# Performance work log

Hardware: AMD Instinct MI355X
Metric: run time of the kernel (lower is better)

Reference implementation:

```python
import jax, jax.numpy as jnp
import numpy as np

DECAY = 0.85          # decay_factor
LAM = 0.5             # lambda_diversity
EPS = 1e-12


def setup_inputs() -> dict:
    key = jax.random.key(0)
    ks = jax.random.split(key, 6)
    N, D = 32768, 512
    return {
        "predictions": jax.random.normal(ks[0], (N,), jnp.float32),
        "target_scores": jax.random.normal(ks[1], (N,), jnp.float32),
        "context_embeddings": jax.random.normal(ks[2], (N, D), jnp.float32),
        "input_embeddings": jax.random.normal(ks[3], (N, D), jnp.float32),
        "dsm_embeddings": jax.random.normal(ks[4], (N, D), jnp.float32),
        "explanation_embeddings": jax.random.normal(ks[5], (N, D), jnp.float32),
        "k": 16,
    }


def reference(predictions, target_scores, context_embeddings, input_embeddings,
              dsm_embeddings, explanation_embeddings, k):
    # relevance probabilities over all N candidates (dim=0 softmax as in torch)
    rel = jax.nn.softmax(predictions.squeeze(), axis=0)

    # L2-normalize once so cos_sim is a plain dot product
    E = explanation_embeddings
    En = E / (jnp.linalg.norm(E, axis=-1, keepdims=True) + EPS)  # [N, D]
    N = En.shape[0]

    # Greedy ERR/MMR relevance-diversity selection of k items:
    #   score_t(i) = decay^t * rel[i] - lambda * max_{j in selected} cos(E_i, E_j)
    # pick argmax over unselected; err_score_t = decay^t * rel[selected_t]
    def step(carry, t):
        mask, max_sim = carry                       # [N] bool, [N] f32
        decay = DECAY ** t.astype(rel.dtype)
        score = decay * rel - LAM * max_sim
        score = jnp.where(mask, -jnp.inf, score)
        idx = jnp.argmax(score)
        err = rel[idx] * decay
        sim_new = En @ En[idx]                      # cos sim of all to new pick
        return (mask.at[idx].set(True),
                jnp.maximum(max_sim, sim_new)), (err, idx)

    init = (jnp.zeros((N,), bool), jnp.zeros((N,), rel.dtype))
    _, (errs, sel) = jax.lax.scan(step, init, jnp.arange(k))

    err_loss = -jnp.sum(errs)

    # mmr_loss = -sum_i max_j cos(E_i, E_j) over selected set (self included,
    # exactly as the original code does with util.cos_sim(...).max())
    S = En[sel]                                    # [k, D]
    sims = S @ S.T                                 # [k, k]
    mmr_loss = -jnp.sum(jnp.max(sims, axis=1))

    return err_loss + LAM * mmr_loss
```

## Files before the change

kernel.cpp:

```cpp
#include <hip/hip_runtime.h>
#include <cmath>


#define DECAYF 0.85f
#define LAMF   0.5f
#define EPSF   1e-12f

constexpr int D    = 512;
constexpr int KMAX = 16;
constexpr int NBLK = 256;
constexpr int TPB  = 1024;
constexpr int NW   = TPB / 64;
constexpr int RPW  = 8;
constexpr int RPB  = NW * RPW;

using u32 = unsigned int;
using u64 = unsigned long long;

__device__ inline float wsum(float v) {
#pragma unroll
    for (int o = 32; o > 0; o >>= 1) v += __shfl_xor(v, o);
    return v;
}
__device__ inline float wmaxf(float v) {
#pragma unroll
    for (int o = 32; o > 0; o >>= 1) v = fmaxf(v, __shfl_xor(v, o));
    return v;
}
__device__ inline u64 wmax64(u64 v) {
#pragma unroll
    for (int o = 32; o > 0; o >>= 1) {
        u64 w = __shfl_xor(v, o);
        v = (w > v) ? w : v;
    }
    return v;
}
__device__ inline u32 fkey(float f) {
    u32 u = __float_as_uint(f);
    return (u & 0x80000000u) ? ~u : (u | 0x80000000u);
}
__device__ inline u64 aload(const u64* p) {
    return __hip_atomic_load(p, __ATOMIC_RELAXED, __HIP_MEMORY_SCOPE_AGENT);
}
__device__ inline u64 poll_slot(const u64* p) {
    u64 v = aload(p);
    while (v == 0ull) { __builtin_amdgcn_s_sleep(1); v = aload(p); }
    return v;
}
__device__ inline void publish(u64* p, u64 v) {
    __hip_atomic_store(p, v, __ATOMIC_RELAXED, __HIP_MEMORY_SCOPE_AGENT);
}

__global__ __launch_bounds__(TPB, 4) void fused_kernel(
        const float* __restrict__ pred,
        const float* __restrict__ E,
        const int*   __restrict__ kptr,
        float* __restrict__ out,
        u64*   __restrict__ sm,
        u64*   __restrict__ part,
        int    SL) {
    const int b = blockIdx.x, tid = threadIdx.x;
    const int wv = tid >> 6, lane = tid & 63;

    __shared__ float pred_s[RPB];
    __shared__ u64   scan_s[NBLK];
    __shared__ u64   wkey_s[NW];
    __shared__ float m_s, S_s;
    __shared__ int   j_s;
    __shared__ int   sel_s[KMAX];
    __shared__ float invsel_s[KMAX];
    __shared__ float rmax_s[KMAX];

    int kk = kptr[0];
    if (kk > KMAX) kk = KMAX;
    if (kk < 0) kk = 0;

    if (tid < RPB) pred_s[tid] = pred[b * RPB + tid];
    __syncthreads();
    if (wv == 0) {
        float p0 = pred_s[lane], p1 = pred_s[lane + 64];
        float mb = wmaxf(fmaxf(p0, p1));
        float sb = wsum(expf(p0 - mb) + expf(p1 - mb));
        if (lane == 0)
            publish(&sm[(size_t)b * SL],
                    ((u64)__float_as_uint(mb) << 32) | __float_as_uint(sb));
    }
    asm volatile("" ::: "memory");

    const int row0 = b * RPB + wv * RPW;
    float r[RPW][8];
#pragma unroll
    for (int rr = 0; rr < RPW; ++rr) {
        const float4* p = (const float4*)(E + (size_t)(row0 + rr) * D) + 2 * lane;
        float4 a0 = p[0], a1 = p[1];
        r[rr][0] = a0.x; r[rr][1] = a0.y; r[rr][2] = a0.z; r[rr][3] = a0.w;
        r[rr][4] = a1.x; r[rr][5] = a1.y; r[rr][6] = a1.z; r[rr][7] = a1.w;
        float ss = 0.f;
#pragma unroll
        for (int e = 0; e < 8; ++e) ss += r[rr][e] * r[rr][e];
        ss = wsum(ss);
        float inv = 1.f / (sqrtf(ss) + EPSF);
#pragma unroll
        for (int e = 0; e < 8; ++e) r[rr][e] *= inv;
        asm volatile("" : "+v"(r[rr][0]), "+v"(r[rr][1]), "+v"(r[rr][2]), "+v"(r[rr][3]),
                          "+v"(r[rr][4]), "+v"(r[rr][5]), "+v"(r[rr][6]), "+v"(r[rr][7]));
    }

    if (tid < NBLK) scan_s[tid] = poll_slot(&sm[(size_t)tid * SL]);
    __syncthreads();
    if (wv == 0) {
        u64 v0 = scan_s[lane], v1 = scan_s[lane + 64],
            v2 = scan_s[lane + 128], v3 = scan_s[lane + 192];
        float m0 = __uint_as_float((u32)(v0 >> 32)), m1 = __uint_as_float((u32)(v1 >> 32));
        float m2 = __uint_as_float((u32)(v2 >> 32)), m3 = __uint_as_float((u32)(v3 >> 32));
        float M = wmaxf(fmaxf(fmaxf(m0, m1), fmaxf(m2, m3)));
        float acc = __uint_as_float((u32)(v0 & 0xFFFFFFFFull)) * expf(m0 - M)
                  + __uint_as_float((u32)(v1 & 0xFFFFFFFFull)) * expf(m1 - M)
                  + __uint_as_float((u32)(v2 & 0xFFFFFFFFull)) * expf(m2 - M)
                  + __uint_as_float((u32)(v3 & 0xFFFFFFFFull)) * expf(m3 - M);
        acc = wsum(acc);
        if (lane == 0) { m_s = M; S_s = acc; }
    }
    __syncthreads();
    const float M    = m_s;
    const float Sinv = 1.f / S_s;

    float drel_r[RPW], msim_r[RPW];
#pragma unroll
    for (int rr = 0; rr < RPW; ++rr) {
        drel_r[rr] = expf(pred_s[wv * RPW + rr] - M) * Sinv;
        msim_r[rr] = 0.f;
    }

    int j = -1;
    for (int t = 0; t < KMAX; ++t) {
        if (t >= kk) break;
        if (t > 0) {
            const float4* pj = (const float4*)(E + (size_t)j * D) + 2 * lane;
            float4 b0 = pj[0], b1 = pj[1];
            float bj[8] = {b0.x, b0.y, b0.z, b0.w, b1.x, b1.y, b1.z, b1.w};
            float ss = 0.f;
#pragma unroll
            for (int e = 0; e < 8; ++e) ss += bj[e] * bj[e];
            ss = wsum(ss);
            const float js = 1.f / (sqrtf(ss) + EPSF);
#pragma unroll
            for (int e = 0; e < 8; ++e) bj[e] *= js;
#pragma unroll
            for (int rr = 0; rr < RPW; ++rr) {
                float d = 0.f;
#pragma unroll
                for (int e = 0; e < 8; ++e) d += r[rr][e] * bj[e];
                d = wsum(d);
                msim_r[rr] = (row0 + rr == j) ? INFINITY
                                              : fmaxf(msim_r[rr], d);
            }
        }
        u64 best = 0ull;
#pragma unroll
        for (int rr = 0; rr < RPW; ++rr) {
            const float sc = drel_r[rr] - LAMF * msim_r[rr];
            const u64 key = ((u64)fkey(sc) << 32) | (u32)~(u32)(row0 + rr);
            best = (key > best) ? key : best;
        }
#pragma unroll
        for (int rr = 0; rr < RPW; ++rr) drel_r[rr] *= DECAYF;
        if (lane == 0) wkey_s[wv] = best;
        __syncthreads();
        if (wv == 0) {
            u64 v = (lane < NW) ? wkey_s[lane] : 0ull;
            v = wmax64(v);
            u64* base = part + (size_t)t * NBLK * SL;
            if (lane == 0) publish(&base[(size_t)b * SL], v);
            u64 a0 = 0, a1 = 0, a2 = 0, a3 = 0;
            const u64* s0 = &base[(size_t)(lane      ) * SL];
            const u64* s1 = &base[(size_t)(lane +  64) * SL];
            const u64* s2 = &base[(size_t)(lane + 128) * SL];
            const u64* s3 = &base[(size_t)(lane + 192) * SL];
            for (;;) {
                if (a0 == 0ull) a0 = aload(s0);
                if (a1 == 0ull) a1 = aload(s1);
                if (a2 == 0ull) a2 = aload(s2);
                if (a3 == 0ull) a3 = aload(s3);
                if (a0 != 0ull && a1 != 0ull && a2 != 0ull && a3 != 0ull) break;
                __builtin_amdgcn_s_sleep(1);
            }
            u64 m = (a1 > a0) ? a1 : a0;
            m = (a2 > m) ? a2 : m;
            m = (a3 > m) ? a3 : m;
            m = wmax64(m);
            if (lane == 0) {
                const int jj = (int)~(u32)(m & 0xFFFFFFFFull);
                j_s = jj;
                sel_s[t] = jj;
            }
        }
        __syncthreads();
        j = j_s;
    }

    if (b == 0) {
        for (int ii = wv; ii < kk; ii += NW) {
            const int si = sel_s[ii];
            const float4* pa = (const float4*)(E + (size_t)si * D) + 2 * lane;
            float4 a0 = pa[0], a1 = pa[1];
            float ss = a0.x*a0.x + a0.y*a0.y + a0.z*a0.z + a0.w*a0.w
                     + a1.x*a1.x + a1.y*a1.y + a1.z*a1.z + a1.w*a1.w;
            ss = wsum(ss);
            if (lane == 0) invsel_s[ii] = 1.f / (sqrtf(ss) + EPSF);
        }
        __syncthreads();
        for (int ii = wv; ii < kk; ii += NW) {
            const int si = sel_s[ii];
            const float4* pa = (const float4*)(E + (size_t)si * D) + 2 * lane;
            float4 a0 = pa[0], a1 = pa[1];
            const float ia = invsel_s[ii];
            float av[8] = {a0.x * ia, a0.y * ia, a0.z * ia, a0.w * ia,
                           a1.x * ia, a1.y * ia, a1.z * ia, a1.w * ia};
            float m = -INFINITY;
            for (int jj = 0; jj < kk; ++jj) {
                const float4* pb = (const float4*)(E + (size_t)sel_s[jj] * D) + 2 * lane;
                float4 c0 = pb[0], c1 = pb[1];
                float d = av[0]*c0.x + av[1]*c0.y + av[2]*c0.z + av[3]*c0.w
                        + av[4]*c1.x + av[5]*c1.y + av[6]*c1.z + av[7]*c1.w;
                d = wsum(d);
                m = fmaxf(m, d * invsel_s[jj]);
            }
            if (lane == 0) rmax_s[ii] = m;
        }
        __syncthreads();
        if (tid == 0) {
            float es = 0.f, mm = 0.f;
            for (int t = 0; t < kk; ++t) {
                es += powf(DECAYF, (float)t) * expf(pred[sel_s[t]] - M) * Sinv;
                mm += rmax_s[t];
            }
            out[0] = -es - LAMF * mm;
        }
    }
}

extern "C" void kernel_launch(void* const* d_in, const int* in_sizes, int n_in,
                              void* d_out, int out_size, void* d_ws, size_t ws_size,
                              hipStream_t stream) {
    const float* pred = (const float*)d_in[0];
    const float* E    = (const float*)d_in[5];
    const int*   kptr = (const int*)d_in[6];
    float* out        = (float*)d_out;

    const size_t slots = (size_t)NBLK * (1 + KMAX);
    const int SL = (ws_size >= slots * 16 * sizeof(u64)) ? 16 : 1;
    u64* sm   = (u64*)d_ws;
    u64* part = sm + (size_t)NBLK * SL;
    hipMemsetAsync(d_ws, 0, slots * SL * sizeof(u64), stream);

    void* args[] = {(void*)&pred, (void*)&E, (void*)&kptr, (void*)&out,
                    (void*)&sm, (void*)&part, (void*)&SL};
    hipLaunchCooperativeKernel((const void*)fused_kernel,
                               dim3(NBLK), dim3(TPB), args, 0, stream);
}
```

Measured before the change: 146.5 us.

## Reduce per-step argmax in one block and broadcast via single slot

Previously every block polled all 256 partial slots on each greedy step to compute the global argmax. Now only block 0 gathers and reduces the partials, then publishes the winner to a per-step broadcast slot that all other blocks poll. The padded slot stride (SL) is also dropped in favour of dense packing, which shrinks the memset and workspace. This cuts global polling traffic but adds a second serial hop (gather, then broadcast) to each step's critical path, and dense slots may cause false sharing.

```diff
diff --git a/kernel.cpp b/kernel.cpp
--- a/kernel.cpp
+++ b/kernel.cpp
@@ -58,7 +58,7 @@
         float* __restrict__ out,
         u64*   __restrict__ sm,
         u64*   __restrict__ part,
-        int    SL) {
+        u64*   __restrict__ bcast) {
     const int b = blockIdx.x, tid = threadIdx.x;
     const int wv = tid >> 6, lane = tid & 63;
 
@@ -82,8 +82,7 @@
         float mb = wmaxf(fmaxf(p0, p1));
         float sb = wsum(expf(p0 - mb) + expf(p1 - mb));
         if (lane == 0)
-            publish(&sm[(size_t)b * SL],
-                    ((u64)__float_as_uint(mb) << 32) | __float_as_uint(sb));
+            publish(&sm[b], ((u64)__float_as_uint(mb) << 32) | __float_as_uint(sb));
     }
     asm volatile("" ::: "memory");
 
@@ -106,7 +105,7 @@
                           "+v"(r[rr][4]), "+v"(r[rr][5]), "+v"(r[rr][6]), "+v"(r[rr][7]));
     }
 
-    if (tid < NBLK) scan_s[tid] = poll_slot(&sm[(size_t)tid * SL]);
+    if (tid < NBLK) scan_s[tid] = poll_slot(&sm[tid]);
     __syncthreads();
     if (wv == 0) {
         u64 v0 = scan_s[lane], v1 = scan_s[lane + 64],
@@ -170,27 +169,26 @@
         if (wv == 0) {
             u64 v = (lane < NW) ? wkey_s[lane] : 0ull;
             v = wmax64(v);
-            u64* base = part + (size_t)t * NBLK * SL;
-            if (lane == 0) publish(&base[(size_t)b * SL], v);
-            u64 a0 = 0, a1 = 0, a2 = 0, a3 = 0;
-            const u64* s0 = &base[(size_t)(lane      ) * SL];
-            const u64* s1 = &base[(size_t)(lane +  64) * SL];
-            const u64* s2 = &base[(size_t)(lane + 128) * SL];
-            const u64* s3 = &base[(size_t)(lane + 192) * SL];
-            for (;;) {
-                if (a0 == 0ull) a0 = aload(s0);
-                if (a1 == 0ull) a1 = aload(s1);
-                if (a2 == 0ull) a2 = aload(s2);
-                if (a3 == 0ull) a3 = aload(s3);
-                if (a0 != 0ull && a1 != 0ull && a2 != 0ull && a3 != 0ull) break;
-                __builtin_amdgcn_s_sleep(1);
-            }
-            u64 m = (a1 > a0) ? a1 : a0;
-            m = (a2 > m) ? a2 : m;
-            m = (a3 > m) ? a3 : m;
-            m = wmax64(m);
+            u64* base = part + (size_t)t * NBLK;
+            if (lane == 0) publish(&base[b], v);
+            if (b == 0) {
+                u64 a0 = 0, a1 = 0, a2 = 0, a3 = 0;
+                for (;;) {
+                    if (a0 == 0ull) a0 = aload(&base[lane]);
+                    if (a1 == 0ull) a1 = aload(&base[lane + 64]);
+                    if (a2 == 0ull) a2 = aload(&base[lane + 128]);
+                    if (a3 == 0ull) a3 = aload(&base[lane + 192]);
+                    if (a0 && a1 && a2 && a3) break;
+                    __builtin_amdgcn_s_sleep(1);
+                }
+                u64 m = (a1 > a0) ? a1 : a0;
+                m = (a2 > m) ? a2 : m;
+                m = (a3 > m) ? a3 : m;
+                m = wmax64(m);
+                if (lane == 0) publish(&bcast[t], m);
+            }
             if (lane == 0) {
-                const int jj = (int)~(u32)(m & 0xFFFFFFFFull);
+                const int jj = (int)~(u32)(poll_slot(&bcast[t]) & 0xFFFFFFFFull);
                 j_s = jj;
                 sel_s[t] = jj;
             }
@@ -248,14 +246,13 @@
     const int*   kptr = (const int*)d_in[6];
     float* out        = (float*)d_out;
 
-    const size_t slots = (size_t)NBLK * (1 + KMAX);
-    const int SL = (ws_size >= slots * 16 * sizeof(u64)) ? 16 : 1;
-    u64* sm   = (u64*)d_ws;
-    u64* part = sm + (size_t)NBLK * SL;
-    hipMemsetAsync(d_ws, 0, slots * SL * sizeof(u64), stream);
+    u64* sm    = (u64*)d_ws;
+    u64* part  = sm + NBLK;
+    u64* bcast = part + (size_t)KMAX * NBLK;
+    hipMemsetAsync(d_ws, 0, (NBLK + KMAX * NBLK + KMAX) * sizeof(u64), stream);
 
     void* args[] = {(void*)&pred, (void*)&E, (void*)&kptr, (void*)&out,
-                    (void*)&sm, (void*)&part, (void*)&SL};
+                    (void*)&sm, (void*)&part, (void*)&bcast};
     hipLaunchCooperativeKernel((const void*)fused_kernel,
                                dim3(NBLK), dim3(TPB), args, 0, stream);
 }
```

New measurement: 137.2 us. -6.3%, faster.
